# Kernel optimization log

Hardware: AMD Instinct MI355X
Metric: run time of the kernel (lower is better)

Reference implementation:

```python
import jax, jax.numpy as jnp
import numpy as np

N, E = 50000, 800000
F_IN, F_HID, F_OUT = 128, 128, 64


def sage_conv(x, src, dst, Wl, bl, Wr, n_nodes):
    # gather source features, scatter-mean to destination nodes
    msg = x[src]                                                # [E, F]
    agg = jax.ops.segment_sum(msg, dst, num_segments=n_nodes)   # [N, F]
    cnt = jax.ops.segment_sum(jnp.ones((src.shape[0], 1), x.dtype), dst,
                              num_segments=n_nodes)             # [N, 1]
    agg = agg / jnp.maximum(cnt, 1.0)                           # mean; isolated nodes -> 0
    return agg @ Wl + bl + x @ Wr


def setup_inputs() -> dict:
    key = jax.random.key(0)
    ks = jax.random.split(key, 12)
    x = jax.random.normal(ks[0], (N, F_IN), dtype=jnp.float32)
    edge_index = jax.random.randint(ks[1], (2, E), 0, N, dtype=jnp.int64)

    def glorot(k, shape):
        lim = float(np.sqrt(6.0 / (shape[0] + shape[1])))
        return jax.random.uniform(k, shape, jnp.float32, -lim, lim)

    dims = [(F_IN, F_HID), (F_HID, F_HID), (F_HID, F_OUT)]
    params = {}
    for i, (fi, fo) in enumerate(dims):
        params[f"Wl{i}"] = glorot(ks[2 + 3 * i], (fi, fo))
        params[f"bl{i}"] = jnp.zeros((fo,), jnp.float32)
        params[f"Wr{i}"] = glorot(ks[3 + 3 * i], (fi, fo))
    return {"x": x, "edge_index": edge_index, **params}


def reference(x, edge_index, Wl0, bl0, Wr0, Wl1, bl1, Wr1, Wl2, bl2, Wr2):
    src, dst = edge_index[0], edge_index[1]
    layers = [(Wl0, bl0, Wr0), (Wl1, bl1, Wr1), (Wl2, bl2, Wr2)]
    h = x
    for i, (Wl, bl, Wr) in enumerate(layers):
        h = sage_conv(h, src, dst, Wl, bl, Wr, N)
        if i < len(layers) - 1:
            h = jax.nn.elu(h)  # dropout is identity in eval mode
    return jax.nn.log_softmax(h, axis=1)
```

## Files before the change

### kernel.cpp

```cpp
#include <hip/hip_runtime.h>
#include <hip/hip_bf16.h>

#define NN 50000
#define NE 800000
#define NPAD 50048
#define NBK 512
#define RNG 98
#define BCAP 2560
#define CSTRIDE 16
#define EPB 4096
#define NFB ((NE + EPB - 1) / EPB)
#define GB (NPAD / 64)
#define GB2 (NPAD / 32)
#define CSRCAP2 768

typedef __attribute__((ext_vector_type(8))) short bf8;
typedef __attribute__((ext_vector_type(4))) float f4;
typedef __attribute__((ext_vector_type(2))) float f2v;
typedef __attribute__((ext_vector_type(4))) unsigned int u4v;
typedef __attribute__((ext_vector_type(2))) unsigned int u2v;

__device__ __forceinline__ unsigned short f2bf(float f) {
    union { float f; unsigned int u; } x; x.f = f;
    unsigned int r = x.u + 0x7fffu + ((x.u >> 16) & 1u);
    return (unsigned short)(r >> 16);
}
__device__ __forceinline__ float b2f(short s) {
    union { unsigned int u; float f; } x;
    x.u = ((unsigned int)(unsigned short)s) << 16;
    return x.f;
}
__device__ __forceinline__ unsigned char f2fp8(float v) {
    return (unsigned char)(__builtin_amdgcn_cvt_pk_fp8_f32(v, v, 0, false) & 0xff);
}
__device__ __forceinline__ void acc16_fp8(f2v* acc, u4v v) {
    #pragma unroll
    for (int t = 0; t < 4; ++t) {
        acc[2 * t]     += __builtin_amdgcn_cvt_pk_f32_fp8((int)v[t], false);
        acc[2 * t + 1] += __builtin_amdgcn_cvt_pk_f32_fp8((int)v[t], true);
    }
}
__device__ __forceinline__ void acc8_fp8(f2v* acc, u2v v) {
    #pragma unroll
    for (int t = 0; t < 2; ++t) {
        acc[2 * t]     += __builtin_amdgcn_cvt_pk_f32_fp8((int)v[t], false);
        acc[2 * t + 1] += __builtin_amdgcn_cvt_pk_f32_fp8((int)v[t], true);
    }
}

__global__ void zero_k(int* __restrict__ cursor, int* __restrict__ rowptr) {
    cursor[threadIdx.x * CSTRIDE] = 0;
    if (threadIdx.x == 0) rowptr[NN] = NE;
}

__global__ __launch_bounds__(256) void prep_k(const int* __restrict__ ei,
                                              int* __restrict__ cursor,
                                              unsigned int* __restrict__ bucket,
                                              const float* __restrict__ Wl0, const float* __restrict__ Wr0,
                                              const float* __restrict__ Wl1, const float* __restrict__ Wr1,
                                              const float* __restrict__ Wl2, const float* __restrict__ Wr2,
                                              unsigned short* __restrict__ Bp) {
    __shared__ unsigned int sorted[EPB];
    __shared__ unsigned short sbuck[EPB];
    __shared__ int hist[NBK], ofs[NBK], gpos[NBK], stmp[256];
    const int tid = threadIdx.x;
    if (blockIdx.x >= NFB) {
        int idx = (blockIdx.x - NFB) * 256 + tid;
        const float *Wl, *Wr;
        int Mo, local;
        unsigned short* out;
        if (idx < 32768)       { Wl = Wl0; Wr = Wr0; Mo = 128; out = Bp;         local = idx; }
        else if (idx < 65536)  { Wl = Wl1; Wr = Wr1; Mo = 128; out = Bp + 32768; local = idx - 32768; }
        else if (idx < 81920)  { Wl = Wl2; Wr = Wr2; Mo = 64;  out = Bp + 65536; local = idx - 65536; }
        else return;
        int ncol = 2 * Mo;
        int k = local / ncol, c = local % ncol;
        float v = (c < Mo) ? Wl[k * Mo + c] : Wr[k * Mo + (c - Mo)];
        int cf = c >> 4, ks = k >> 5;
        int lane = (c & 15) | (((k & 31) >> 3) << 4);
        int i = k & 7;
        out[(((cf << 2) | ks) * 64 + lane) * 8 + i] = f2bf(v);
        return;
    }
    const int e0 = blockIdx.x * EPB;
    const int n = (NE - e0) < EPB ? (NE - e0) : EPB;

    for (int i = tid; i < NBK; i += 256) hist[i] = 0;
    __syncthreads();

    unsigned int ent[EPB / 256];
    short bks[EPB / 256];
    #pragma unroll
    for (int j = 0; j < EPB / 256; ++j) {
        const int li = tid + j * 256;
        int b = -1; unsigned v = 0;
        if (li < n) {
            const int e = e0 + li;
            const int s = ei[e];
            const int d = ei[NE + e];
            b = d / RNG;
            v = (unsigned)s | ((unsigned)(d - b * RNG) << 16);
            atomicAdd(&hist[b], 1);
        }
        ent[j] = v; bks[j] = (short)b;
    }
    __syncthreads();

    const int p0 = hist[2 * tid], p1 = hist[2 * tid + 1];
    stmp[tid] = p0 + p1;
    __syncthreads();
    #pragma unroll
    for (int off = 1; off < 256; off <<= 1) {
        const int t = (tid >= off) ? stmp[tid - off] : 0;
        __syncthreads();
        stmp[tid] += t;
        __syncthreads();
    }
    const int pbase = stmp[tid] - p0 - p1;
    ofs[2 * tid] = pbase;
    ofs[2 * tid + 1] = pbase + p0;
    __syncthreads();

    for (int i = tid; i < NBK; i += 256) {
        const int c = hist[i];
        gpos[i] = c ? atomicAdd(&cursor[i * CSTRIDE], c) : 0;
    }
    for (int i = tid; i < NBK; i += 256) hist[i] = ofs[i];
    __syncthreads();
    #pragma unroll
    for (int j = 0; j < EPB / 256; ++j) {
        if (bks[j] >= 0) {
            const int r = atomicAdd(&hist[(int)bks[j]], 1);
            sorted[r] = ent[j];
            sbuck[r] = (unsigned short)bks[j];
        }
    }
    __syncthreads();
    for (int i = tid; i < n; i += 256) {
        const int b = sbuck[i];
        const int idx = gpos[b] + (i - ofs[b]);
        if (idx < BCAP) bucket[(size_t)b * BCAP + idx] = sorted[i];
    }
}

__global__ __launch_bounds__(256) void mid_k(const unsigned int* __restrict__ bucket,
                                             const int* __restrict__ cursor,
                                             int* __restrict__ rowptr, int* __restrict__ csr,
                                             const float* __restrict__ x,
                                             const unsigned short* __restrict__ Bp,
                                             unsigned char* __restrict__ Yq,
                                             unsigned short* __restrict__ Z) {
    __shared__ unsigned int ent[BCAP];
    __shared__ int hist[RNG], lcur[RNG], sofs[NBK], stmp[256];
    const int tid = threadIdx.x;
    if (blockIdx.x < NBK) {
        const int b = blockIdx.x;
        const int c0 = cursor[(2 * tid) * CSTRIDE];
        const int c1 = cursor[(2 * tid + 1) * CSTRIDE];
        stmp[tid] = c0 + c1;
        __syncthreads();
        #pragma unroll
        for (int off = 1; off < 256; off <<= 1) {
            const int t = (tid >= off) ? stmp[tid - off] : 0;
            __syncthreads();
            stmp[tid] += t;
            __syncthreads();
        }
        const int pbase = stmp[tid] - c0 - c1;
        sofs[2 * tid] = pbase;
        sofs[2 * tid + 1] = pbase + c0;
        for (int i = tid; i < RNG; i += 256) { hist[i] = 0; lcur[i] = 0; }
        __syncthreads();

        const int sz0 = cursor[b * CSTRIDE];
        const int sz = sz0 < BCAP ? sz0 : BCAP;
        const int gbase = sofs[b];
        for (int i = tid; i < sz; i += 256) {
            unsigned v = bucket[(size_t)b * BCAP + i];
            ent[i] = v;
            atomicAdd(&hist[v >> 16], 1);
        }
        __syncthreads();
        if (tid == 0) {
            int acc = 0;
            #pragma unroll 2
            for (int i = 0; i < RNG; ++i) { int c = hist[i]; hist[i] = acc; acc += c; }
        }
        __syncthreads();
        const int n0 = b * RNG;
        for (int i = tid; i < RNG; i += 256) {
            int nn = n0 + i;
            if (nn < NN) rowptr[nn] = gbase + hist[i];
        }
        for (int i = tid; i < sz; i += 256) {
            unsigned v = ent[i];
            int dloc = v >> 16;
            int r = atomicAdd(&lcur[dloc], 1);
            csr[gbase + hist[dloc] + r] = (int)(v & 0xffffu);
        }
        return;
    }
    const int wave = tid >> 6;
    const int lane = tid & 63;
    const int r0 = (blockIdx.x - NBK) * 64;

    bf8 bfr[4][4];
    const bf8* bp = reinterpret_cast<const bf8*>(Bp);
    #pragma unroll
    for (int cf = 0; cf < 4; ++cf)
        #pragma unroll
        for (int ks = 0; ks < 4; ++ks)
            bfr[cf][ks] = bp[((wave * 4 + cf) * 4 + ks) * 64 + lane];

    const int rlane = lane & 15, kc = lane >> 4;
    #pragma unroll
    for (int rf = 0; rf < 4; ++rf) {
        const int arow = r0 + rf * 16 + rlane;
        const bool ok = arow < NN;
        const float4* ap = reinterpret_cast<const float4*>(x + (size_t)arow * 128);
        bf8 afr[4];
        #pragma unroll
        for (int ks = 0; ks < 4; ++ks) {
            float4 a0 = make_float4(0.f,0.f,0.f,0.f), a1 = a0;
            if (ok) { a0 = ap[ks * 8 + kc * 2]; a1 = ap[ks * 8 + kc * 2 + 1]; }
            bf8 t;
            t[0]=(short)f2bf(a0.x); t[1]=(short)f2bf(a0.y); t[2]=(short)f2bf(a0.z); t[3]=(short)f2bf(a0.w);
            t[4]=(short)f2bf(a1.x); t[5]=(short)f2bf(a1.y); t[6]=(short)f2bf(a1.z); t[7]=(short)f2bf(a1.w);
            afr[ks] = t;
        }
        f4 acc[4];
        #pragma unroll
        for (int cf = 0; cf < 4; ++cf) acc[cf] = (f4){0.f, 0.f, 0.f, 0.f};
        #pragma unroll
        for (int ks = 0; ks < 4; ++ks)
            #pragma unroll
            for (int cf = 0; cf < 4; ++cf)
                acc[cf] = __builtin_amdgcn_mfma_f32_16x16x32_bf16(afr[ks], bfr[cf][ks], acc[cf], 0, 0, 0);
        const int orow0 = r0 + rf * 16 + (lane >> 4) * 4;
        #pragma unroll
        for (int j = 0; j < 4; ++j) {
            const int orow = orow0 + j;
            if (orow < NN) {
                #pragma unroll
                for (int cf = 0; cf < 4; ++cf) {
                    const int col = (wave * 4 + cf) * 16 + rlane;
                    const float v = acc[cf][j];
                    if (col < 128) Yq[(size_t)orow * 128 + col] = f2fp8(v);
                    else           Z[(size_t)orow * 128 + (col - 128)] = f2bf(v);
                }
            }
        }
    }
}

__global__ __launch_bounds__(256) void perm_k(const int* __restrict__ rowptr,
                                              int* __restrict__ perm) {
    const int w = (int)((blockIdx.x * 256 + threadIdx.x) >> 6);
    const int lane = threadIdx.x & 63;
    if (w >= GB2) return;
    const int n0 = w * 32;
    const int i = lane & 31;
    const int n = n0 + i;
    const int deg = (n < NN) ? (rowptr[n + 1] - rowptr[n]) : -1;
    int rank = 0;
    #pragma unroll
    for (int j = 0; j < 32; ++j) {
        const int dj = __shfl(deg, j, 64);
        rank += (dj > deg) || (dj == deg && j < i);
    }
    if (lane < 32) perm[w * 32 + rank] = i;
}

template<int MOUT>
__global__ __launch_bounds__(256) void fused_k(const int* __restrict__ rowptr,
                                               const int* __restrict__ csr,
                                               const int* __restrict__ perm,
                                               const unsigned char* __restrict__ Yq_in,
                                               const unsigned short* __restrict__ Z_in,
                                               const float* __restrict__ bias,
                                               const unsigned short* __restrict__ Bp,
                                               unsigned char* __restrict__ Yq_out,
                                               unsigned short* __restrict__ Z_out) {
    constexpr int CFW = 2 * MOUT / 64;
    __shared__ int lcsr[CSRCAP2];
    __shared__ unsigned short tile[32 * 128];
    const int tid = threadIdx.x;
    const int n0 = blockIdx.x * 32;
    const int nend = (n0 + 32 > NN) ? NN : (n0 + 32);
    const int beg0 = rowptr[n0];
    const int tot = rowptr[nend] - beg0;
    const bool inlds = tot <= CSRCAP2;
    if (inlds) for (int i = tid; i < tot; i += 256) lcsr[i] = csr[beg0 + i];
    __syncthreads();

    const int gp = perm[blockIdx.x * 32 + (tid >> 3)];
    const int l = tid & 7;
    const int node = n0 + gp;
    char* tbase = reinterpret_cast<char*>(tile);
    if (node < NN) {
        const int beg = rowptr[node], end = rowptr[node + 1];
        f2v acc[8];
        #pragma unroll
        for (int i = 0; i < 8; ++i) acc[i] = (f2v){0.f, 0.f};
        int e = beg;
        for (; e + 8 <= end; e += 8) {
            int ss[8];
            #pragma unroll
            for (int j = 0; j < 8; ++j) ss[j] = inlds ? lcsr[e + j - beg0] : csr[e + j];
            u4v u[8];
            #pragma unroll
            for (int j = 0; j < 8; ++j)
                u[j] = *reinterpret_cast<const u4v*>(Yq_in + (size_t)ss[j] * 128 + l * 16);
            #pragma unroll
            for (int j = 0; j < 8; ++j) acc16_fp8(acc, u[j]);
        }
        for (; e + 4 <= end; e += 4) {
            int ss[4];
            #pragma unroll
            for (int j = 0; j < 4; ++j) ss[j] = inlds ? lcsr[e + j - beg0] : csr[e + j];
            u4v u[4];
            #pragma unroll
            for (int j = 0; j < 4; ++j)
                u[j] = *reinterpret_cast<const u4v*>(Yq_in + (size_t)ss[j] * 128 + l * 16);
            #pragma unroll
            for (int j = 0; j < 4; ++j) acc16_fp8(acc, u[j]);
        }
        for (; e < end; ++e) {
            const int s0 = inlds ? lcsr[e - beg0] : csr[e];
            acc16_fp8(acc, *reinterpret_cast<const u4v*>(Yq_in + (size_t)s0 * 128 + l * 16));
        }
        const float invd = 1.0f / fmaxf((float)(end - beg), 1.0f);
        const bf8* zp = reinterpret_cast<const bf8*>(&Z_in[(size_t)node * 128 + l * 16]);
        const float* bp = bias + l * 16;
        #pragma unroll
        for (int c8 = 0; c8 < 2; ++c8) {
            const bf8 z = zp[c8];
            bf8 o;
            #pragma unroll
            for (int i = 0; i < 8; ++i) {
                const int k = c8 * 8 + i;
                float h = acc[k >> 1][k & 1] * invd + b2f(z[i]) + bp[c8 * 8 + i];
                h = h > 0.f ? h : expf(h) - 1.f;
                o[i] = (short)f2bf(h);
            }
            const unsigned byte = (unsigned)((gp * 256 + l * 32 + c8 * 16) ^ ((gp & 7) << 4));
            *reinterpret_cast<bf8*>(tbase + byte) = o;
        }
    } else {
        const bf8 zz = (bf8){0,0,0,0,0,0,0,0};
        #pragma unroll
        for (int c8 = 0; c8 < 2; ++c8) {
            const unsigned byte = (unsigned)((gp * 256 + l * 32 + c8 * 16) ^ ((gp & 7) << 4));
            *reinterpret_cast<bf8*>(tbase + byte) = zz;
        }
    }

    const int wave = tid >> 6;
    const int lane = tid & 63;
    bf8 bfr[CFW][4];
    const bf8* bpf = reinterpret_cast<const bf8*>(Bp);
    #pragma unroll
    for (int cf = 0; cf < CFW; ++cf)
        #pragma unroll
        for (int ks = 0; ks < 4; ++ks)
            bfr[cf][ks] = bpf[((wave * CFW + cf) * 4 + ks) * 64 + lane];
    __syncthreads();

    const int rlane = lane & 15, kc = lane >> 4;
    #pragma unroll
    for (int rf = 0; rf < 2; ++rf) {
        const int row = rf * 16 + rlane;
        bf8 afr[4];
        #pragma unroll
        for (int ks = 0; ks < 4; ++ks) {
            const unsigned byte = (unsigned)((row * 256 + ks * 64 + kc * 16) ^ ((row & 7) << 4));
            afr[ks] = *reinterpret_cast<const bf8*>(tbase + byte);
        }
        f4 acc[CFW];
        #pragma unroll
        for (int cf = 0; cf < CFW; ++cf) acc[cf] = (f4){0.f, 0.f, 0.f, 0.f};
        #pragma unroll
        for (int ks = 0; ks < 4; ++ks)
            #pragma unroll
            for (int cf = 0; cf < CFW; ++cf)
                acc[cf] = __builtin_amdgcn_mfma_f32_16x16x32_bf16(afr[ks], bfr[cf][ks], acc[cf], 0, 0, 0);
        const int orow0 = n0 + rf * 16 + (lane >> 4) * 4;
        #pragma unroll
        for (int j = 0; j < 4; ++j) {
            const int orow = orow0 + j;
            if (orow < NN) {
                #pragma unroll
                for (int cf = 0; cf < CFW; ++cf) {
                    const int col = (wave * CFW + cf) * 16 + rlane;
                    const float v = acc[cf][j];
                    if (col < MOUT) Yq_out[(size_t)orow * MOUT + col] = f2fp8(v);
                    else            Z_out[(size_t)orow * MOUT + (col - MOUT)] = f2bf(v);
                }
            }
        }
    }
}

__global__ __launch_bounds__(256) void gathlsm_k(const int* __restrict__ rowptr,
                                                 const int* __restrict__ csr,
                                                 const int* __restrict__ perm,
                                                 const unsigned char* __restrict__ Yq2,
                                                 const unsigned short* __restrict__ Z2,
                                                 const float* __restrict__ bias,
                                                 float* __restrict__ lout) {
    __shared__ int lcsr[CSRCAP2];
    const int tid = threadIdx.x;
    const int n0 = blockIdx.x * 32;
    const int nend = (n0 + 32 > NN) ? NN : (n0 + 32);
    const int beg0 = rowptr[n0];
    const int tot = rowptr[nend] - beg0;
    const bool inlds = tot <= CSRCAP2;
    if (inlds) for (int i = tid; i < tot; i += 256) lcsr[i] = csr[beg0 + i];
    __syncthreads();

    const int gp = perm[blockIdx.x * 32 + (tid >> 3)];
    const int l = tid & 7;
    const int n = n0 + gp;
    if (n >= NN) return;
    const int beg = rowptr[n], end = rowptr[n + 1];

    f2v acc[4];
    #pragma unroll
    for (int i = 0; i < 4; ++i) acc[i] = (f2v){0.f, 0.f};
    int e = beg;
    for (; e + 8 <= end; e += 8) {
        int ss[8];
        #pragma unroll
        for (int j = 0; j < 8; ++j) ss[j] = inlds ? lcsr[e + j - beg0] : csr[e + j];
        u2v u[8];
        #pragma unroll
        for (int j = 0; j < 8; ++j)
            u[j] = *reinterpret_cast<const u2v*>(Yq2 + (size_t)ss[j] * 64 + l * 8);
        #pragma unroll
        for (int j = 0; j < 8; ++j) acc8_fp8(acc, u[j]);
    }
    for (; e < end; ++e) {
        const int s0 = inlds ? lcsr[e - beg0] : csr[e];
        acc8_fp8(acc, *reinterpret_cast<const u2v*>(Yq2 + (size_t)s0 * 64 + l * 8));
    }
    const float inv = 1.0f / fmaxf((float)(end - beg), 1.0f);
    const bf8 z = *reinterpret_cast<const bf8*>(&Z2[(size_t)n * 64 + l * 8]);
    float h[8];
    #pragma unroll
    for (int i = 0; i < 8; ++i) h[i] = acc[i >> 1][i & 1] * inv + b2f(z[i]) + bias[l * 8 + i];

    float m = h[0];
    #pragma unroll
    for (int i = 1; i < 8; ++i) m = fmaxf(m, h[i]);
    m = fmaxf(m, __shfl_xor(m, 1, 64));
    m = fmaxf(m, __shfl_xor(m, 2, 64));
    m = fmaxf(m, __shfl_xor(m, 4, 64));
    float s = 0.f;
    #pragma unroll
    for (int i = 0; i < 8; ++i) s += expf(h[i] - m);
    s += __shfl_xor(s, 1, 64);
    s += __shfl_xor(s, 2, 64);
    s += __shfl_xor(s, 4, 64);
    const float lg = m + logf(s);
    float* op = &lout[(size_t)n * 64 + l * 8];
    float4 o0, o1;
    o0.x = h[0] - lg; o0.y = h[1] - lg; o0.z = h[2] - lg; o0.w = h[3] - lg;
    o1.x = h[4] - lg; o1.y = h[5] - lg; o1.z = h[6] - lg; o1.w = h[7] - lg;
    *reinterpret_cast<float4*>(op) = o0;
    *reinterpret_cast<float4*>(op + 4) = o1;
}

extern "C" void kernel_launch(void* const* d_in, const int* in_sizes, int n_in,
                              void* d_out, int out_size, void* d_ws, size_t ws_size,
                              hipStream_t stream) {
    const float* x   = (const float*)d_in[0];
    const int*   ei  = (const int*)d_in[1];
    const float* Wl0 = (const float*)d_in[2];
    const float* bl0 = (const float*)d_in[3];
    const float* Wr0 = (const float*)d_in[4];
    const float* Wl1 = (const float*)d_in[5];
    const float* bl1 = (const float*)d_in[6];
    const float* Wr1 = (const float*)d_in[7];
    const float* Wl2 = (const float*)d_in[8];
    const float* bl2 = (const float*)d_in[9];
    const float* Wr2 = (const float*)d_in[10];
    float* out = (float*)d_out;

    unsigned char*  Yqa = (unsigned char*)d_ws;
    unsigned char*  Yqb = Yqa + (size_t)NPAD * 128;
    unsigned short* Za  = (unsigned short*)(Yqb + (size_t)NPAD * 128);
    unsigned short* Zb  = Za + (size_t)NPAD * 128;
    unsigned short* Bp  = Zb + (size_t)NPAD * 128;
    int* rowptr = (int*)(Bp + 81920);
    int* cursor = rowptr + (NN + 2);
    int* csr    = cursor + NBK * CSTRIDE;
    unsigned int* bucket = (unsigned int*)(csr + NE);
    int* perm   = (int*)(bucket + (size_t)NBK * BCAP);

    zero_k<<<1, NBK, 0, stream>>>(cursor, rowptr);
    prep_k<<<NFB + 320, 256, 0, stream>>>(ei, cursor, bucket, Wl0, Wr0, Wl1, Wr1, Wl2, Wr2, Bp);
    mid_k<<<NBK + GB, 256, 0, stream>>>(bucket, cursor, rowptr, csr, x, Bp, Yqa, Za);
    perm_k<<<(GB2 * 64 + 255) / 256, 256, 0, stream>>>(rowptr, perm);
    fused_k<128><<<GB2, 256, 0, stream>>>(rowptr, csr, perm, Yqa, Za, bl0, Bp + 32768, Yqb, Zb);
    fused_k<64><<<GB2, 256, 0, stream>>>(rowptr, csr, perm, Yqb, Zb, bl1, Bp + 65536, Yqa, Za);
    gathlsm_k<<<GB2, 256, 0, stream>>>(rowptr, csr, perm, Yqa, Za, bl2, out);
}
```

Baseline: 125.1 us.

## Split fused gather-GEMM and final layer into single-wave blocks of 8 nodes

Rewrites the per-layer fused gather+MFMA kernel and the final log-softmax kernel to use 64-thread single-wave blocks, each handling 8 nodes of a degree-sorted 32-node group. The LDS staging of CSR indices and the shared block barrier are removed, and self-feature loads are hoisted before the gather loop. Each wave now computes all output columns for a 16-row MFMA tile of which only 8 rows are real, with the rest zero-padded, and writes rows through the permutation. The aim is finer-grained scheduling and less waiting on the slowest node in a block, at the cost of wasted MFMA rows and more weight-fragment loads per node.

```diff
diff --git a/kernel.cpp b/kernel.cpp
--- a/kernel.cpp
+++ b/kernel.cpp
@@ -12,7 +12,7 @@
 #define NFB ((NE + EPB - 1) / EPB)
 #define GB (NPAD / 64)
 #define GB2 (NPAD / 32)
-#define CSRCAP2 768
+#define GB8 (NPAD / 8)
 
 typedef __attribute__((ext_vector_type(8))) short bf8;
 typedef __attribute__((ext_vector_type(4))) float f4;
@@ -272,33 +272,40 @@
 }
 
 template<int MOUT>
-__global__ __launch_bounds__(256) void fused_k(const int* __restrict__ rowptr,
-                                               const int* __restrict__ csr,
-                                               const int* __restrict__ perm,
-                                               const unsigned char* __restrict__ Yq_in,
-                                               const unsigned short* __restrict__ Z_in,
-                                               const float* __restrict__ bias,
-                                               const unsigned short* __restrict__ Bp,
-                                               unsigned char* __restrict__ Yq_out,
-                                               unsigned short* __restrict__ Z_out) {
-    constexpr int CFW = 2 * MOUT / 64;
-    __shared__ int lcsr[CSRCAP2];
-    __shared__ unsigned short tile[32 * 128];
-    const int tid = threadIdx.x;
-    const int n0 = blockIdx.x * 32;
-    const int nend = (n0 + 32 > NN) ? NN : (n0 + 32);
-    const int beg0 = rowptr[n0];
-    const int tot = rowptr[nend] - beg0;
-    const bool inlds = tot <= CSRCAP2;
-    if (inlds) for (int i = tid; i < tot; i += 256) lcsr[i] = csr[beg0 + i];
-    __syncthreads();
-
-    const int gp = perm[blockIdx.x * 32 + (tid >> 3)];
-    const int l = tid & 7;
-    const int node = n0 + gp;
+__global__ __launch_bounds__(64, 4) void fused_k(const int* __restrict__ rowptr,
+                                                 const int* __restrict__ csr,
+                                                 const int* __restrict__ perm,
+                                                 const unsigned char* __restrict__ Yq_in,
+                                                 const unsigned short* __restrict__ Z_in,
+                                                 const float* __restrict__ bias,
+                                                 const unsigned short* __restrict__ Bp,
+                                                 unsigned char* __restrict__ Yq_out,
+                                                 unsigned short* __restrict__ Z_out) {
+    constexpr int NCF = 2 * MOUT / 16;
+    __shared__ unsigned short tile[16 * 128];
+    const int lane = threadIdx.x;
+    const int t = blockIdx.x >> 2;
+    const int c = blockIdx.x & 3;
+    const int n0p = t * 32;
+    const int g = lane >> 3;
+    const int l = lane & 7;
+    const int gp = perm[t * 32 + c * 8 + g];
+    const int node = n0p + gp;
     char* tbase = reinterpret_cast<char*>(tile);
+
+    {
+        const bf8 zz = (bf8){0,0,0,0,0,0,0,0};
+        #pragma unroll
+        for (int c8 = 0; c8 < 2; ++c8) {
+            const unsigned byte = (unsigned)(((g + 8) * 256 + l * 32 + c8 * 16) ^ (((g + 8) & 7) << 4));
+            *reinterpret_cast<bf8*>(tbase + byte) = zz;
+        }
+    }
+
     if (node < NN) {
         const int beg = rowptr[node], end = rowptr[node + 1];
+        const bf8* zp = reinterpret_cast<const bf8*>(&Z_in[(size_t)node * 128 + l * 16]);
+        const bf8 z0 = zp[0], z1 = zp[1];
         f2v acc[8];
         #pragma unroll
         for (int i = 0; i < 8; ++i) acc[i] = (f2v){0.f, 0.f};
@@ -306,7 +313,7 @@
         for (; e + 8 <= end; e += 8) {
             int ss[8];
             #pragma unroll
-            for (int j = 0; j < 8; ++j) ss[j] = inlds ? lcsr[e + j - beg0] : csr[e + j];
+            for (int j = 0; j < 8; ++j) ss[j] = csr[e + j];
             u4v u[8];
             #pragma unroll
             for (int j = 0; j < 8; ++j)
@@ -317,7 +324,7 @@
         for (; e + 4 <= end; e += 4) {
             int ss[4];
             #pragma unroll
-            for (int j = 0; j < 4; ++j) ss[j] = inlds ? lcsr[e + j - beg0] : csr[e + j];
+            for (int j = 0; j < 4; ++j) ss[j] = csr[e + j];
             u4v u[4];
             #pragma unroll
             for (int j = 0; j < 4; ++j)
@@ -326,73 +333,66 @@
             for (int j = 0; j < 4; ++j) acc16_fp8(acc, u[j]);
         }
         for (; e < end; ++e) {
-            const int s0 = inlds ? lcsr[e - beg0] : csr[e];
+            const int s0 = csr[e];
             acc16_fp8(acc, *reinterpret_cast<const u4v*>(Yq_in + (size_t)s0 * 128 + l * 16));
         }
         const float invd = 1.0f / fmaxf((float)(end - beg), 1.0f);
-        const bf8* zp = reinterpret_cast<const bf8*>(&Z_in[(size_t)node * 128 + l * 16]);
         const float* bp = bias + l * 16;
         #pragma unroll
         for (int c8 = 0; c8 < 2; ++c8) {
-            const bf8 z = zp[c8];
+            const bf8 z = c8 ? z1 : z0;
             bf8 o;
             #pragma unroll
             for (int i = 0; i < 8; ++i) {
                 const int k = c8 * 8 + i;
-                float h = acc[k >> 1][k & 1] * invd + b2f(z[i]) + bp[c8 * 8 + i];
+                float h = acc[k >> 1][k & 1] * invd + b2f(z[i]) + bp[k];
                 h = h > 0.f ? h : expf(h) - 1.f;
                 o[i] = (short)f2bf(h);
             }
-            const unsigned byte = (unsigned)((gp * 256 + l * 32 + c8 * 16) ^ ((gp & 7) << 4));
+            const unsigned byte = (unsigned)((g * 256 + l * 32 + c8 * 16) ^ ((g & 7) << 4));
             *reinterpret_cast<bf8*>(tbase + byte) = o;
         }
     } else {
         const bf8 zz = (bf8){0,0,0,0,0,0,0,0};
         #pragma unroll
         for (int c8 = 0; c8 < 2; ++c8) {
-            const unsigned byte = (unsigned)((gp * 256 + l * 32 + c8 * 16) ^ ((gp & 7) << 4));
+            const unsigned byte = (unsigned)((g * 256 + l * 32 + c8 * 16) ^ ((g & 7) << 4));
             *reinterpret_cast<bf8*>(tbase + byte) = zz;
         }
     }
-
-    const int wave = tid >> 6;
-    const int lane = tid & 63;
-    bf8 bfr[CFW][4];
+    __syncthreads();
+
+    const int rlane = lane & 15, kc = lane >> 4;
+    const int row = rlane;
+    bf8 afr[4];
+    #pragma unroll
+    for (int ks = 0; ks < 4; ++ks) {
+        const unsigned byte = (unsigned)((row * 256 + ks * 64 + kc * 16) ^ ((row & 7) << 4));
+        afr[ks] = *reinterpret_cast<const bf8*>(tbase + byte);
+    }
+    const int rbase = kc * 4;
+    int permv[4] = {0, 0, 0, 0};
+    if (rbase < 8) {
+        #pragma unroll
+        for (int j = 0; j < 4; ++j) permv[j] = perm[t * 32 + c * 8 + rbase + j];
+    }
     const bf8* bpf = reinterpret_cast<const bf8*>(Bp);
     #pragma unroll
-    for (int cf = 0; cf < CFW; ++cf)
+    for (int cf = 0; cf < NCF; ++cf) {
+        bf8 bfr[4];
+        #pragma unroll
+        for (int ks = 0; ks < 4; ++ks) bfr[ks] = bpf[(cf * 4 + ks) * 64 + lane];
+        f4 acc = (f4){0.f, 0.f, 0.f, 0.f};
         #pragma unroll
         for (int ks = 0; ks < 4; ++ks)
-            bfr[cf][ks] = bpf[((wave * CFW + cf) * 4 + ks) * 64 + lane];
-    __syncthreads();
-
-    const int rlane = lane & 15, kc = lane >> 4;
-    #pragma unroll
-    for (int rf = 0; rf < 2; ++rf) {
-        const int row = rf * 16 + rlane;
-        bf8 afr[4];
-        #pragma unroll
-        for (int ks = 0; ks < 4; ++ks) {
-            const unsigned byte = (unsigned)((row * 256 + ks * 64 + kc * 16) ^ ((row & 7) << 4));
-            afr[ks] = *reinterpret_cast<const bf8*>(tbase + byte);
-        }
-        f4 acc[CFW];
-        #pragma unroll
-        for (int cf = 0; cf < CFW; ++cf) acc[cf] = (f4){0.f, 0.f, 0.f, 0.f};
-        #pragma unroll
-        for (int ks = 0; ks < 4; ++ks)
-            #pragma unroll
-            for (int cf = 0; cf < CFW; ++cf)
-                acc[cf] = __builtin_amdgcn_mfma_f32_16x16x32_bf16(afr[ks], bfr[cf][ks], acc[cf], 0, 0, 0);
-        const int orow0 = n0 + rf * 16 + (lane >> 4) * 4;
-        #pragma unroll
-        for (int j = 0; j < 4; ++j) {
-            const int orow = orow0 + j;
-            if (orow < NN) {
-                #pragma unroll
-                for (int cf = 0; cf < CFW; ++cf) {
-                    const int col = (wave * CFW + cf) * 16 + rlane;
-                    const float v = acc[cf][j];
+            acc = __builtin_amdgcn_mfma_f32_16x16x32_bf16(afr[ks], bfr[ks], acc, 0, 0, 0);
+        if (rbase < 8) {
+            const int col = cf * 16 + rlane;
+            #pragma unroll
+            for (int j = 0; j < 4; ++j) {
+                const int orow = n0p + permv[j];
+                if (orow < NN) {
+                    const float v = acc[j];
                     if (col < MOUT) Yq_out[(size_t)orow * MOUT + col] = f2fp8(v);
                     else            Z_out[(size_t)orow * MOUT + (col - MOUT)] = f2bf(v);
                 }
@@ -401,29 +401,24 @@
     }
 }
 
-__global__ __launch_bounds__(256) void gathlsm_k(const int* __restrict__ rowptr,
-                                                 const int* __restrict__ csr,
-                                                 const int* __restrict__ perm,
-                                                 const unsigned char* __restrict__ Yq2,
-                                                 const unsigned short* __restrict__ Z2,
-                                                 const float* __restrict__ bias,
-                                                 float* __restrict__ lout) {
-    __shared__ int lcsr[CSRCAP2];
-    const int tid = threadIdx.x;
-    const int n0 = blockIdx.x * 32;
-    const int nend = (n0 + 32 > NN) ? NN : (n0 + 32);
-    const int beg0 = rowptr[n0];
-    const int tot = rowptr[nend] - beg0;
-    const bool inlds = tot <= CSRCAP2;
-    if (inlds) for (int i = tid; i < tot; i += 256) lcsr[i] = csr[beg0 + i];
-    __syncthreads();
-
-    const int gp = perm[blockIdx.x * 32 + (tid >> 3)];
-    const int l = tid & 7;
-    const int n = n0 + gp;
+__global__ __launch_bounds__(64, 4) void gathlsm_k(const int* __restrict__ rowptr,
+                                                   const int* __restrict__ csr,
+                                                   const int* __restrict__ perm,
+                                                   const unsigned char* __restrict__ Yq2,
+                                                   const unsigned short* __restrict__ Z2,
+                                                   const float* __restrict__ bias,
+                                                   float* __restrict__ lout) {
+    const int lane = threadIdx.x;
+    const int t = blockIdx.x >> 2;
+    const int c = blockIdx.x & 3;
+    const int g = lane >> 3;
+    const int l = lane & 7;
+    const int gp = perm[t * 32 + c * 8 + g];
+    const int n = t * 32 + gp;
     if (n >= NN) return;
     const int beg = rowptr[n], end = rowptr[n + 1];
 
+    const bf8 z = *reinterpret_cast<const bf8*>(&Z2[(size_t)n * 64 + l * 8]);
     f2v acc[4];
     #pragma unroll
     for (int i = 0; i < 4; ++i) acc[i] = (f2v){0.f, 0.f};
@@ -431,7 +426,7 @@
     for (; e + 8 <= end; e += 8) {
         int ss[8];
         #pragma unroll
-        for (int j = 0; j < 8; ++j) ss[j] = inlds ? lcsr[e + j - beg0] : csr[e + j];
+        for (int j = 0; j < 8; ++j) ss[j] = csr[e + j];
         u2v u[8];
         #pragma unroll
         for (int j = 0; j < 8; ++j)
@@ -440,11 +435,10 @@
         for (int j = 0; j < 8; ++j) acc8_fp8(acc, u[j]);
     }
     for (; e < end; ++e) {
-        const int s0 = inlds ? lcsr[e - beg0] : csr[e];
+        const int s0 = csr[e];
         acc8_fp8(acc, *reinterpret_cast<const u2v*>(Yq2 + (size_t)s0 * 64 + l * 8));
     }
     const float inv = 1.0f / fmaxf((float)(end - beg), 1.0f);
-    const bf8 z = *reinterpret_cast<const bf8*>(&Z2[(size_t)n * 64 + l * 8]);
     float h[8];
     #pragma unroll
     for (int i = 0; i < 8; ++i) h[i] = acc[i >> 1][i & 1] * inv + b2f(z[i]) + bias[l * 8 + i];
@@ -501,7 +495,7 @@
     prep_k<<<NFB + 320, 256, 0, stream>>>(ei, cursor, bucket, Wl0, Wr0, Wl1, Wr1, Wl2, Wr2, Bp);
     mid_k<<<NBK + GB, 256, 0, stream>>>(bucket, cursor, rowptr, csr, x, Bp, Yqa, Za);
     perm_k<<<(GB2 * 64 + 255) / 256, 256, 0, stream>>>(rowptr, perm);
-    fused_k<128><<<GB2, 256, 0, stream>>>(rowptr, csr, perm, Yqa, Za, bl0, Bp + 32768, Yqb, Zb);
-    fused_k<64><<<GB2, 256, 0, stream>>>(rowptr, csr, perm, Yqb, Zb, bl1, Bp + 65536, Yqa, Za);
-    gathlsm_k<<<GB2, 256, 0, stream>>>(rowptr, csr, perm, Yqa, Za, bl2, out);
-}
+    fused_k<128><<<GB8, 64, 0, stream>>>(rowptr, csr, perm, Yqa, Za, bl0, Bp + 32768, Yqb, Zb);
+    fused_k<64><<<GB8, 64, 0, stream>>>(rowptr, csr, perm, Yqb, Zb, bl1, Bp + 65536, Yqa, Za);
+    gathlsm_k<<<GB8, 64, 0, stream>>>(rowptr, csr, perm, Yqa, Za, bl2, out);
+}
```

After: 147.5 us. 1.18x slower.
